# Performance work log

Hardware: AMD Instinct MI355X
Metric: run time of the kernel (lower is better)

Reference implementation:

```python
import jax, jax.numpy as jnp
import numpy as np

B, N, D = 8, 2048, 768
H = 12
HD = D // H
W = 16          # window_size
HOP = 8         # hop_size
GB = N // 2 + 1   # global freq bins = 1025
LB = W // 2 + 1   # local freq bins = 9
NW = (N - W) // HOP + 1  # num windows = 255
EPS_LN = 1e-5


def setup_inputs() -> dict:
    key = jax.random.key(0)
    ks = jax.random.split(key, 12)
    s = 0.02
    return {
        "x": jax.random.normal(ks[0], (B, N, D), dtype=jnp.float32),
        "base_filter_global": jnp.ones((H, GB, 1), jnp.float32),
        "base_filter_local": jnp.ones((H, LB, 1), jnp.float32),
        "modrelu_bias_global": jnp.full((H, GB, 1), -0.1, jnp.float32),
        "modrelu_bias_local": jnp.full((H, LB, 1), -0.1, jnp.float32),
        "w1g": jax.random.normal(ks[1], (D, D), jnp.float32) * s,
        "b1g": jnp.zeros((D,), jnp.float32),
        "w2g": jax.random.normal(ks[2], (D, H * GB), jnp.float32) * s,
        "b2g": jnp.zeros((H * GB,), jnp.float32),
        "w1l": jax.random.normal(ks[3], (D, D), jnp.float32) * s,
        "b1l": jnp.zeros((D,), jnp.float32),
        "w2l": jax.random.normal(ks[4], (D, H * LB), jnp.float32) * s,
        "b2l": jnp.zeros((H * LB,), jnp.float32),
        "fusion_w": jax.random.normal(ks[5], (2,), jnp.float32) * 0.5,
        "ln_gamma": jnp.ones((D,), jnp.float32),
        "ln_beta": jnp.zeros((D,), jnp.float32),
    }


def _modrelu(z, bias):
    # modReLU: ReLU(|z| + b) * z / |z|  (|z| clamped at 1e-6 in denominator)
    a = jnp.abs(z)
    return z * (jax.nn.relu(a + bias) / jnp.maximum(a, 1e-6))


def _hann(w):
    # torch.hann_window default (periodic=True)
    n = jnp.arange(w, dtype=jnp.float32)
    return 0.5 * (1.0 - jnp.cos(2.0 * jnp.pi * n / w))


def reference(x, base_filter_global, base_filter_local, modrelu_bias_global,
              modrelu_bias_local, w1g, b1g, w2g, b2g, w1l, b1l, w2l, b2l,
              fusion_w, ln_gamma, ln_beta):
    b, n, d = x.shape
    x_heads = x.reshape(b, n, H, HD).transpose(0, 2, 1, 3)  # (B,H,N,hd)

    # ---- global branch ----
    Fg = jnp.fft.rfft(x_heads, axis=2, norm='ortho')  # (B,H,GB,hd) complex
    ctx = x.mean(axis=1)  # (B,D)
    mg = jnp.tanh(jax.nn.gelu(ctx @ w1g + b1g, approximate=False) @ w2g + b2g)
    mg = mg.reshape(b, H, GB, 1)
    Fg = Fg * (base_filter_global[None] + mg)
    Fg = _modrelu(Fg, modrelu_bias_global[None])
    x_global = jnp.fft.irfft(Fg, n=n, axis=2, norm='ortho')  # (B,H,N,hd)

    # ---- local (STFT) branch ----
    idx = jnp.arange(NW)[:, None] * HOP + jnp.arange(W)[None, :]  # (NW,W)
    x_win = x_heads[:, :, idx, :]  # (B,H,NW,W,hd)
    w = _hann(W)[None, None, None, :, None]
    x_win = x_win * w
    Fl = jnp.fft.rfft(x_win, axis=3, norm='ortho')  # (B,H,NW,LB,hd)
    ml = jnp.tanh(jax.nn.gelu(ctx @ w1l + b1l, approximate=False) @ w2l + b2l)
    ml = ml.reshape(b, H, 1, LB, 1)
    Fl = Fl * (base_filter_local[None, :, None] + ml)
    Fl = _modrelu(Fl, modrelu_bias_local[None, :, None])
    x_lwin = jnp.fft.irfft(Fl, n=W, axis=3, norm='ortho') * w  # (B,H,NW,W,hd)

    # vectorized overlap-add
    flat_idx = idx.reshape(-1)  # (NW*W,)
    x_local = jnp.zeros((b, H, n, HD), x.dtype).at[:, :, flat_idx, :].add(
        x_lwin.reshape(b, H, NW * W, HD))

    # ---- fuse + residual + layernorm ----
    fused = x_global * fusion_w[0] + x_local * fusion_w[1]  # Linear(2,1,bias=False)
    x_out = fused.transpose(0, 2, 1, 3).reshape(b, n, d)
    y = x + x_out  # dropout is identity at p=0 / eval
    mu = y.mean(axis=-1, keepdims=True)
    var = y.var(axis=-1, keepdims=True)
    return (y - mu) / jnp.sqrt(var + EPS_LN) * ln_gamma + ln_beta
```

## Files before the change

kernel.cpp:

```cpp
#include <hip/hip_runtime.h>
#include <math.h>

#define B_  8
#define N_  2048
#define D_  768
#define H_  12
#define HD_ 64
#define GB_ 1025
#define LB_ 9
#define NW_ 255

#define CBX(i) ((i) + ((i) >> 4))
#define TWX(i) ((i) + ((i) >> 4))

#define C1_ 0.92387953251128674f
#define S1_ 0.38268343236508978f
#define R2_ 0.70710678118654752f

#define FBF(i,k,wr,wi) { const float ar=yr[i],ai=yi[i],br=yr[k],bi=yi[k]; \
  yr[i]=ar+br; yi[i]=ai+bi; const float dr=ar-br, di=ai-bi; \
  yr[k]=fmaf(dr,wr,-(di*(wi))); yi[k]=fmaf(dr,wi,di*(wr)); }
#define FBF1(i,k) { const float ar=yr[i],ai=yi[i],br=yr[k],bi=yi[k]; \
  yr[i]=ar+br; yi[i]=ai+bi; yr[k]=ar-br; yi[k]=ai-bi; }
#define FBFmi(i,k) { const float ar=yr[i],ai=yi[i],br=yr[k],bi=yi[k]; \
  yr[i]=ar+br; yi[i]=ai+bi; yr[k]=ai-bi; yi[k]=br-ar; }

#define IBF(i,k,wr,wi) { const float br=yr[k],bi=yi[k]; \
  const float tr=fmaf(br,wr,-(bi*(wi))), ti=fmaf(br,wi,bi*(wr)); \
  yr[k]=yr[i]-tr; yi[k]=yi[i]-ti; yr[i]+=tr; yi[i]+=ti; }
#define IBF1(i,k) { const float tr=yr[k], ti=yi[k]; \
  yr[k]=yr[i]-tr; yi[k]=yi[i]-ti; yr[i]+=tr; yi[i]+=ti; }
#define IBFpi(i,k) { const float tr=-yi[k], ti=yr[k]; \
  yr[k]=yr[i]-tr; yi[k]=yi[i]-ti; yr[i]+=tr; yi[i]+=ti; }

__device__ __forceinline__ float2 cmulf(float2 a, float2 b) {
  return make_float2(fmaf(a.x, b.x, -(a.y*b.y)), fmaf(a.x, b.y, a.y*b.x));
}
__device__ __forceinline__ float2 csqf(float2 a){ return make_float2(fmaf(a.x,a.x,-(a.y*a.y)), 2.0f*a.x*a.y); }

__device__ __forceinline__ float4 dadd(float4 a, float4 b){ return make_float4(a.x+b.x,a.y+b.y,a.z+b.z,a.w+b.w); }
__device__ __forceinline__ float4 dsub(float4 a, float4 b){ return make_float4(a.x-b.x,a.y-b.y,a.z-b.z,a.w-b.w); }
__device__ __forceinline__ float4 dmul(float4 a, float2 w){
  return make_float4(fmaf(a.x,w.x,-(a.y*w.y)), fmaf(a.x,w.y,a.y*w.x),
                     fmaf(a.z,w.x,-(a.w*w.y)), fmaf(a.z,w.y,a.w*w.x));
}
__device__ __forceinline__ float4 dmulc(float4 a, float2 w){
  return make_float4(fmaf(a.x,w.x,a.y*w.y), fmaf(a.y,w.x,-(a.x*w.y)),
                     fmaf(a.z,w.x,a.w*w.y), fmaf(a.w,w.x,-(a.z*w.y)));
}
__device__ __forceinline__ float4 dmuli(float4 a){
  return make_float4(a.y, -a.x, a.w, -a.z);
}
__device__ __forceinline__ float4 dmulpi(float4 a){
  return make_float4(-a.y, a.x, -a.w, a.z);
}

__device__ __forceinline__ void mr2(float& ar, float& ai, float filt, float bias){
  ar *= filt; ai *= filt;
  const float a = __builtin_amdgcn_sqrtf(fmaf(ar,ar,ai*ai));
  const float s = fmaxf(a + bias, 0.0f) * __builtin_amdgcn_rcpf(fmaxf(a, 1e-6f));
  ar *= s; ai *= s;
}
__device__ __forceinline__ void mr1(float& v, float filt, float bias){
  v *= filt;
  const float a = fabsf(v);
  v *= fmaxf(a + bias, 0.0f) * __builtin_amdgcn_rcpf(fmaxf(a, 1e-6f));
}

template<int S, int L>
__device__ __forceinline__ void fft_trip_fwd(float4* cb, const float2* tw, int j) {
  const int r    = j & (S-1);
  const int base = r + ((j >> L) << (L+3));
  float4 v[8];
  #pragma unroll
  for (int k = 0; k < 8; ++k) v[k] = cb[CBX(base + S*k)];
  const float2 w = tw[TWX(r * (256/S))];
  const float2 c8 = make_float2(R2_, -R2_);
  float2 W1[4];
  W1[0] = w;
  W1[1] = cmulf(w, c8);
  W1[2] = make_float2(w.y, -w.x);
  W1[3] = make_float2(W1[1].y, -W1[1].x);
  #pragma unroll
  for (int k = 0; k < 4; ++k) {
    const float4 u = v[k], t = v[k+4];
    v[k]   = dadd(u, t);
    v[k+4] = dmul(dsub(u, t), W1[k]);
  }
  const float2 w2  = csqf(w);
  const float2 w2i = make_float2(w2.y, -w2.x);
  {
    float4 d;
    d = dsub(v[0], v[2]); v[0] = dadd(v[0], v[2]); v[2] = dmul(d, w2);
    d = dsub(v[1], v[3]); v[1] = dadd(v[1], v[3]); v[3] = dmul(d, w2i);
    d = dsub(v[4], v[6]); v[4] = dadd(v[4], v[6]); v[6] = dmul(d, w2);
    d = dsub(v[5], v[7]); v[5] = dadd(v[5], v[7]); v[7] = dmul(d, w2i);
  }
  const float2 w4 = csqf(w2);
  #pragma unroll
  for (int k = 0; k < 8; k += 2) {
    const float4 d = dsub(v[k], v[k+1]);
    v[k]   = dadd(v[k], v[k+1]);
    v[k+1] = dmul(d, w4);
  }
  #pragma unroll
  for (int k = 0; k < 8; ++k) cb[CBX(base + S*k)] = v[k];
}

__device__ __forceinline__ void fft_trip4_fwd(float4* cb, int j) {
  const int base = j << 3;
  float4 v[8];
  #pragma unroll
  for (int k = 0; k < 8; ++k) v[k] = cb[CBX(base + k)];
  float4 d;
  d = dsub(v[0], v[2]); v[0] = dadd(v[0], v[2]); v[2] = d;
  d = dsub(v[1], v[3]); v[1] = dadd(v[1], v[3]); v[3] = dmuli(d);
  d = dsub(v[4], v[6]); v[4] = dadd(v[4], v[6]); v[6] = d;
  d = dsub(v[5], v[7]); v[5] = dadd(v[5], v[7]); v[7] = dmuli(d);
  #pragma unroll
  for (int k = 0; k < 8; k += 2) {
    d = dsub(v[k], v[k+1]);
    v[k]   = dadd(v[k], v[k+1]);
    v[k+1] = d;
  }
  #pragma unroll
  for (int k = 0; k < 8; ++k) cb[CBX(base + k)] = v[k];
}

__device__ __forceinline__ void fft_trip1_inv(float4* cb, int j) {
  const int base = j << 3;
  float4 v[8];
  #pragma unroll
  for (int k = 0; k < 8; ++k) v[k] = cb[CBX(base + k)];
  #pragma unroll
  for (int k = 0; k < 8; k += 2) {
    const float4 t = v[k+1];
    v[k+1] = dsub(v[k], t);
    v[k]   = dadd(v[k], t);
  }
  {
    float4 t;
    t = v[2];          v[2] = dsub(v[0], t); v[0] = dadd(v[0], t);
    t = dmulpi(v[3]);  v[3] = dsub(v[1], t); v[1] = dadd(v[1], t);
    t = v[6];          v[6] = dsub(v[4], t); v[4] = dadd(v[4], t);
    t = dmulpi(v[7]);  v[7] = dsub(v[5], t); v[5] = dadd(v[5], t);
  }
  #pragma unroll
  for (int k = 0; k < 8; ++k) cb[CBX(base + k)] = v[k];
}

template<int S, int L>
__device__ __forceinline__ void fft_trip_inv(float4* cb, const float2* tw, int j) {
  const int r    = j & (S-1);
  const int base = r + ((j >> L) << (L+3));
  float4 v[8];
  #pragma unroll
  for (int k = 0; k < 8; ++k) v[k] = cb[CBX(base + S*k)];
  const float2 w  = tw[TWX(r * (256/S))];
  const float2 w2 = csqf(w);
  const float2 w4 = csqf(w2);
  #pragma unroll
  for (int k = 0; k < 8; k += 2) {
    const float4 t = dmulc(v[k+1], w4);
    v[k+1] = dsub(v[k], t);
    v[k]   = dadd(v[k], t);
  }
  {
    float4 t;
    t = dmulc(v[2], w2);          v[2] = dsub(v[0], t); v[0] = dadd(v[0], t);
    t = dmulpi(dmulc(v[3], w2));  v[3] = dsub(v[1], t); v[1] = dadd(v[1], t);
    t = dmulc(v[6], w2);          v[6] = dsub(v[4], t); v[4] = dadd(v[4], t);
    t = dmulpi(dmulc(v[7], w2));  v[7] = dsub(v[5], t); v[5] = dadd(v[5], t);
  }
  const float2 c8 = make_float2(R2_, -R2_);
  float2 W1[4];
  W1[0] = w;
  W1[1] = cmulf(w, c8);
  W1[2] = make_float2(w.y, -w.x);
  W1[3] = make_float2(W1[1].y, -W1[1].x);
  #pragma unroll
  for (int k = 0; k < 4; ++k) {
    const float4 t = dmulc(v[k+4], W1[k]);
    v[k+4] = dsub(v[k], t);
    v[k]   = dadd(v[k], t);
  }
  #pragma unroll
  for (int k = 0; k < 8; ++k) cb[CBX(base + S*k)] = v[k];
}

template<int HALF>
__device__ __forceinline__ void local_path(const float4* cb, const float* lf, const float* lb,
                                           int tid, float* w1a, float* w2a) {
  const float HWIN[16] = {0.0f, 0.038060233744356624f, 0.14644660940672624f, 0.30865828381745508f,
                          0.5f, 0.69134171618254492f, 0.85355339059327376f, 0.96193976625564337f,
                          1.0f, 0.96193976625564337f, 0.85355339059327376f, 0.69134171618254492f,
                          0.5f, 0.30865828381745508f, 0.14644660940672624f, 0.038060233744356624f};
  if (tid < NW_) {
    float yr[16], yi[16];
    #pragma unroll
    for (int t = 0; t < 16; ++t) {
      const float4 v = cb[CBX(tid*8 + t)];
      yr[t] = (HALF ? v.z : v.x) * HWIN[t];
      yi[t] = (HALF ? v.w : v.y) * HWIN[t];
    }
    FBF1(0,8); FBF(1,9,C1_,-S1_); FBF(2,10,R2_,-R2_); FBF(3,11,S1_,-C1_);
    FBFmi(4,12); FBF(5,13,-S1_,-C1_); FBF(6,14,-R2_,-R2_); FBF(7,15,-C1_,-S1_);
    FBF1(0,4); FBF(1,5,R2_,-R2_); FBFmi(2,6); FBF(3,7,-R2_,-R2_);
    FBF1(8,12); FBF(9,13,R2_,-R2_); FBFmi(10,14); FBF(11,15,-R2_,-R2_);
    FBF1(0,2); FBFmi(1,3); FBF1(4,6); FBFmi(5,7);
    FBF1(8,10); FBFmi(9,11); FBF1(12,14); FBFmi(13,15);
    FBF1(0,1); FBF1(2,3); FBF1(4,5); FBF1(6,7);
    FBF1(8,9); FBF1(10,11); FBF1(12,13); FBF1(14,15);
    {
      const int IA[9] = {0,8,4,12,2,10,6,14,1};
      const int IB[9] = {0,15,7,11,3,13,5,9,1};
      #pragma unroll
      for (int l = 0; l <= 8; ++l) {
        const int ia = IA[l], ib = IB[l];
        const float Zar=yr[ia], Zai=yi[ia], Zbr=yr[ib], Zbi=yi[ib];
        float f1r = 0.125f*(Zar+Zbr), f1i = 0.125f*(Zai-Zbi);
        float f2r = 0.125f*(Zai+Zbi), f2i = 0.125f*(Zbr-Zar);
        const float ft = lf[l], bs = lb[l];
        mr2(f1r, f1i, ft, bs);
        mr2(f2r, f2i, ft, bs);
        yr[ia] = f1r - f2i; yi[ia] = f1i + f2r;
        if (l >= 1 && l <= 7) { yr[ib] = f1r + f2i; yi[ib] = f2r - f1i; }
      }
    }
    IBF1(0,1); IBF1(2,3); IBF1(4,5); IBF1(6,7);
    IBF1(8,9); IBF1(10,11); IBF1(12,13); IBF1(14,15);
    IBF1(0,2); IBFpi(1,3); IBF1(4,6); IBFpi(5,7);
    IBF1(8,10); IBFpi(9,11); IBF1(12,14); IBFpi(13,15);
    IBF1(0,4); IBF(1,5,R2_,R2_); IBFpi(2,6); IBF(3,7,-R2_,R2_);
    IBF1(8,12); IBF(9,13,R2_,R2_); IBFpi(10,14); IBF(11,15,-R2_,R2_);
    IBF1(0,8); IBF(1,9,C1_,S1_); IBF(2,10,R2_,R2_); IBF(3,11,S1_,C1_);
    IBFpi(4,12); IBF(5,13,-S1_,C1_); IBF(6,14,-R2_,R2_); IBF(7,15,-C1_,S1_);
    #pragma unroll
    for (int t = 0; t < 16; ++t) {
      const float q = 0.25f * HWIN[t];
      w1a[t] = yr[t] * q;
      w2a[t] = yi[t] * q;
    }
  } else {
    #pragma unroll
    for (int t = 0; t < 16; ++t) { w1a[t] = 0.0f; w2a[t] = 0.0f; }
  }
}

__device__ __forceinline__ void combine_oa(const float* w1a, const float* w2a,
                                           const float (*t1)[8], const float (*t2)[8],
                                           int lane, int wvi, float* r1, float* r2) {
  #pragma unroll
  for (int s = 0; s < 8; ++s) {
    float p1 = __shfl_up(w1a[s+8], 1, 64);
    float p2 = __shfl_up(w2a[s+8], 1, 64);
    if (lane == 0) {
      p1 = wvi ? t1[wvi-1][s] : 0.0f;
      p2 = wvi ? t2[wvi-1][s] : 0.0f;
    }
    r1[s] = w1a[s] + p1;
    r2[s] = w2a[s] + p2;
  }
}

__global__ __launch_bounds__(256) void k_ctx(const float* __restrict__ x,
                                             float* __restrict__ ctx) {
  const int b = blockIdx.x;
  const int nc = blockIdx.y;
  const int tid = threadIdx.x;
  const int n0 = nc * 64;
  for (int c = tid; c < D_; c += 256) {
    float s = 0.0f;
    #pragma unroll 4
    for (int n = 0; n < 64; ++n)
      s += x[((size_t)(b*N_ + n0 + n))*D_ + c];
    atomicAdd(&ctx[b*D_ + c], s);
  }
}

__global__ __launch_bounds__(256) void k_mlp1(
    const float* __restrict__ ctx,
    const float* __restrict__ w1g, const float* __restrict__ b1g,
    const float* __restrict__ w1l, const float* __restrict__ b1l,
    float* __restrict__ h1g, float* __restrict__ h1l) {
  __shared__ float hs[B_*D_];
  __shared__ float red[4][16][33];
  const int tid = threadIdx.x;
  const bool isl = (blockIdx.y != 0);
  const float* w1 = isl ? w1l : w1g;
  const float* b1 = isl ? b1l : b1g;
  float*       h1 = isl ? h1l : h1g;
  const int j0 = (int)blockIdx.x * 64;

  for (int i = tid; i < B_*D_; i += 256) hs[i] = ctx[i] * (1.0f/(float)N_);
  __syncthreads();

  const int jg    = tid & 15;
  const int slice = tid >> 4;
  const int j     = j0 + jg*4;
  float acc[8][4] = {};
  {
    const float4* w14 = (const float4*)w1;
    const int jc = j >> 2;
    const int i0 = slice*48;
    #pragma unroll 4
    for (int ii = 0; ii < 48; ++ii) {
      const int i = i0 + ii;
      const float4 w = w14[(size_t)i*192 + jc];
      #pragma unroll
      for (int b = 0; b < 8; ++b) {
        const float hv = hs[b*D_ + i];
        acc[b][0] = fmaf(hv, w.x, acc[b][0]);
        acc[b][1] = fmaf(hv, w.y, acc[b][1]);
        acc[b][2] = fmaf(hv, w.z, acc[b][2]);
        acc[b][3] = fmaf(hv, w.w, acc[b][3]);
      }
    }
  }
  #pragma unroll
  for (int b = 0; b < 8; ++b) {
    #pragma unroll
    for (int q = 0; q < 4; ++q) {
      float v = acc[b][q];
      v += __shfl_xor(v, 16, 64);
      v += __shfl_xor(v, 32, 64);
      acc[b][q] = v;
    }
  }
  const int wv = tid >> 6;
  if ((tid & 63) < 16) {
    #pragma unroll
    for (int b = 0; b < 8; ++b)
      #pragma unroll
      for (int q = 0; q < 4; ++q)
        red[wv][jg][b*4+q] = acc[b][q];
  }
  __syncthreads();
  for (int s = tid; s < 512; s += 256) {
    const int jg2 = s >> 5;
    const int v2  = s & 31;
    const int b   = v2 >> 2, q = v2 & 3;
    const int jo  = j0 + jg2*4 + q;
    const float sum = red[0][jg2][v2] + red[1][jg2][v2]
                    + red[2][jg2][v2] + red[3][jg2][v2];
    const float v = sum + b1[jo];
    h1[(size_t)b*D_ + jo] = 0.5f * v * (1.0f + erff(v * 0.70710678118654752f));
  }
}

__global__ __launch_bounds__(256) void k_mlp2(
    const float* __restrict__ h1g, const float* __restrict__ h1l,
    const float* __restrict__ w2g, const float* __restrict__ b2g,
    const float* __restrict__ w2l, const float* __restrict__ b2l,
    float* __restrict__ mg, float* __restrict__ ml) {
  __shared__ float hs[B_*D_];
  __shared__ float red[4][16][33];
  const int tid = threadIdx.x;
  const bool isg = (blockIdx.x < 193);
  const float* h1 = isg ? h1g : h1l;
  const float* w2 = isg ? w2g : w2l;
  const float* b2 = isg ? b2g : b2l;
  float*       mo = isg ? mg  : ml;
  const int Jmax = isg ? (H_*GB_) : (H_*LB_);
  const int j0   = isg ? (int)blockIdx.x*64 : ((int)blockIdx.x-193)*64;

  for (int i = tid; i < B_*D_; i += 256) hs[i] = h1[i];
  __syncthreads();

  const int jg    = tid & 15;
  const int slice = tid >> 4;
  const int j     = j0 + jg*4;
  float acc[8][4] = {};
  if (j < Jmax) {
    const float4* w24 = (const float4*)w2;
    const int jc   = j >> 2;
    const int rowq = Jmax >> 2;
    const int i0   = slice*48;
    #pragma unroll 4
    for (int ii = 0; ii < 48; ++ii) {
      const int i = i0 + ii;
      const float4 w = w24[(size_t)i*rowq + jc];
      #pragma unroll
      for (int b = 0; b < 8; ++b) {
        const float hv = hs[b*D_ + i];
        acc[b][0] = fmaf(hv, w.x, acc[b][0]);
        acc[b][1] = fmaf(hv, w.y, acc[b][1]);
        acc[b][2] = fmaf(hv, w.z, acc[b][2]);
        acc[b][3] = fmaf(hv, w.w, acc[b][3]);
      }
    }
  }
  #pragma unroll
  for (int b = 0; b < 8; ++b) {
    #pragma unroll
    for (int q = 0; q < 4; ++q) {
      float v = acc[b][q];
      v += __shfl_xor(v, 16, 64);
      v += __shfl_xor(v, 32, 64);
      acc[b][q] = v;
    }
  }
  const int wv = tid >> 6;
  if ((tid & 63) < 16) {
    #pragma unroll
    for (int b = 0; b < 8; ++b)
      #pragma unroll
      for (int q = 0; q < 4; ++q)
        red[wv][jg][b*4+q] = acc[b][q];
  }
  __syncthreads();
  for (int s = tid; s < 512; s += 256) {
    const int jg2 = s >> 5;
    const int v2  = s & 31;
    const int b   = v2 >> 2, q = v2 & 3;
    const int jo  = j0 + jg2*4 + q;
    if (jo < Jmax) {
      const float sum = red[0][jg2][v2] + red[1][jg2][v2]
                      + red[2][jg2][v2] + red[3][jg2][v2];
      mo[(size_t)b*Jmax + jo] = tanhf(sum + b2[jo]);
    }
  }
}

__global__ __launch_bounds__(256) void k_spectral(
    const float* __restrict__ x,
    const float* __restrict__ bfg, const float* __restrict__ bfl,
    const float* __restrict__ mbg, const float* __restrict__ mbl,
    const float* __restrict__ mg,  const float* __restrict__ ml,
    const float* __restrict__ fw,  float* __restrict__ fused) {
  __shared__ float4 cb[N_ + (N_>>4)];
  __shared__ float2 tw[256 + 16];
  __shared__ float  t1b[2][4][8], t2b[2][4][8];
  __shared__ float  lf[LB_], lb[LB_];

  const int tid = threadIdx.x;
  const int id  = blockIdx.x;
  const int v_  = (id & 7) * 192 + (id >> 3);
  const int dq  = v_ & 15;
  const int bh  = v_ >> 4;
  const int h   = bh % H_;
  const int b   = bh / H_;
  const int d   = dq * 4;
  const int c   = h*HD_ + d;
  const int col0 = bh*HD_ + d;

  {
    float s_, c_;
    sincospif(-(float)tid * (1.0f/1024.0f), &s_, &c_);
    tw[TWX(tid)] = make_float2(c_, s_);
  }
  if (tid < LB_) {
    lf[tid] = bfl[h*LB_ + tid] + ml[(size_t)b*(H_*LB_) + h*LB_ + tid];
    lb[tid] = mbl[h*LB_ + tid];
  }
  for (int n = tid; n < N_; n += 256) {
    cb[CBX(n)] = *(const float4*)&x[((size_t)(b*N_ + n))*D_ + c];
  }
  __syncthreads();

  const int lane = tid & 63, wvi = tid >> 6;
  float r1[8], r2[8], r3[8], r4[8];
  {
    float w1a[16], w2a[16];
    local_path<0>(cb, lf, lb, tid, w1a, w2a);
    if (lane == 63 && tid < NW_) {
      #pragma unroll
      for (int s = 0; s < 8; ++s) { t1b[0][wvi][s] = w1a[8+s]; t2b[0][wvi][s] = w2a[8+s]; }
    }
    __syncthreads();
    combine_oa(w1a, w2a, t1b[0], t2b[0], lane, wvi, r1, r2);
  }
  {
    float w1a[16], w2a[16];
    local_path<1>(cb, lf, lb, tid, w1a, w2a);
    if (lane == 63 && tid < NW_) {
      #pragma unroll
      for (int s = 0; s < 8; ++s) { t1b[1][wvi][s] = w1a[8+s]; t2b[1][wvi][s] = w2a[8+s]; }
    }
    __syncthreads();
    combine_oa(w1a, w2a, t1b[1], t2b[1], lane, wvi, r3, r4);
  }

  fft_trip_fwd<256,8>(cb, tw, tid); __syncthreads();
  fft_trip_fwd< 32,5>(cb, tw, tid); __syncthreads();
  fft_trip_fwd<  4,2>(cb, tw, tid); __syncthreads();
  fft_trip4_fwd(cb, tid);           __syncthreads();

  const float fsc = 0.022097086912079610f;
  {
    const float* mgp = mg + (size_t)b*(H_*GB_) + h*GB_;
    const float* bfp = bfg + h*GB_;
    const float* mbp = mbg + h*GB_;
    const int kb = (tid & 192) + (int)(__brev((unsigned)(tid & 63)) >> 26);
    #pragma unroll
    for (int t = 0; t < 4; ++t) {
      const int k = kb + 256*t;
      if (k == 0) {
        float4 Z0 = cb[CBX(0)], Zn = cb[CBX(1)];
        const float f0t = bfp[0] + mgp[0],     b0 = mbp[0];
        const float fnt = bfp[1024] + mgp[1024], bn = mbp[1024];
        float a0 = Z0.x*fsc, a1 = Z0.y*fsc, a2 = Z0.z*fsc, a3 = Z0.w*fsc;
        mr1(a0, f0t, b0); mr1(a1, f0t, b0); mr1(a2, f0t, b0); mr1(a3, f0t, b0);
        cb[CBX(0)] = make_float4(a0, a1, a2, a3);
        float n0v = Zn.x*fsc, n1v = Zn.y*fsc, n2v = Zn.z*fsc, n3v = Zn.w*fsc;
        mr1(n0v, fnt, bn); mr1(n1v, fnt, bn); mr1(n2v, fnt, bn); mr1(n3v, fnt, bn);
        cb[CBX(1)] = make_float4(n0v, n1v, n2v, n3v);
      } else {
        const int ik  = (int)(__brev((unsigned)k) >> 21);
        const int imk = (int)(__brev((unsigned)(2048 - k)) >> 21);
        const float4 Za = cb[CBX(ik)], Zb = cb[CBX(imk)];
        const float hs_ = 0.5f * fsc;
        const float filt = bfp[k] + mgp[k], bias = mbp[k];
        float f1r = (Za.x + Zb.x) * hs_, f1i = (Za.y - Zb.y) * hs_;
        float f2r = (Za.y + Zb.y) * hs_, f2i = (Zb.x - Za.x) * hs_;
        mr2(f1r, f1i, filt, bias);
        mr2(f2r, f2i, filt, bias);
        float g1r = (Za.z + Zb.z) * hs_, g1i = (Za.w - Zb.w) * hs_;
        float g2r = (Za.w + Zb.w) * hs_, g2i = (Zb.z - Za.z) * hs_;
        mr2(g1r, g1i, filt, bias);
        mr2(g2r, g2i, filt, bias);
        cb[CBX(ik)]  = make_float4(f1r - f2i, f1i + f2r, g1r - g2i, g1i + g2r);
        cb[CBX(imk)] = make_float4(f1r + f2i, f2r - f1i, g1r + g2i, g2r - g1i);
      }
    }
  }
  __syncthreads();

  fft_trip1_inv(cb, tid);           __syncthreads();
  fft_trip_inv<  4,2>(cb, tw, tid); __syncthreads();
  fft_trip_inv< 32,5>(cb, tw, tid); __syncthreads();
  fft_trip_inv<256,8>(cb, tw, tid); __syncthreads();

  const float fw1v = fw[1];
  const float fwg  = fw[0] * fsc;
  float* f0 = fused + (size_t)col0 * N_;
  float* f1p = f0 + N_;
  float* f2p = f0 + 2*N_;
  float* f3p = f0 + 3*N_;
  const int n0 = tid * 8;
  float v0[8], v1[8], v2[8], v3[8];
  #pragma unroll
  for (int s = 0; s < 8; ++s) {
    const float4 g = cb[CBX(n0 + s)];
    v0[s] = fwg * g.x + fw1v * r1[s];
    v1[s] = fwg * g.y + fw1v * r2[s];
    v2[s] = fwg * g.z + fw1v * r3[s];
    v3[s] = fwg * g.w + fw1v * r4[s];
  }
  *(float4*)&f0[n0]    = make_float4(v0[0], v0[1], v0[2], v0[3]);
  *(float4*)&f0[n0+4]  = make_float4(v0[4], v0[5], v0[6], v0[7]);
  *(float4*)&f1p[n0]   = make_float4(v1[0], v1[1], v1[2], v1[3]);
  *(float4*)&f1p[n0+4] = make_float4(v1[4], v1[5], v1[6], v1[7]);
  *(float4*)&f2p[n0]   = make_float4(v2[0], v2[1], v2[2], v2[3]);
  *(float4*)&f2p[n0+4] = make_float4(v2[4], v2[5], v2[6], v2[7]);
  *(float4*)&f3p[n0]   = make_float4(v3[0], v3[1], v3[2], v3[3]);
  *(float4*)&f3p[n0+4] = make_float4(v3[4], v3[5], v3[6], v3[7]);
}

__global__ __launch_bounds__(256) void k_ln(const float* __restrict__ x,
                                            const float* __restrict__ fused,
                                            const float* __restrict__ gamma,
                                            const float* __restrict__ beta,
                                            float* __restrict__ out) {
  __shared__ float yt[16*776];
  __shared__ float mus[16], rsd[16];
  const int bi = blockIdx.x;
  const int b  = bi >> 7;
  const int n0 = (bi & 127) * 16;
  const int tid = threadIdx.x;

  {
    const float4* x4 = (const float4*)(x + ((size_t)(b*N_ + n0))*D_);
    for (int i = tid; i < 16*D_/4; i += 256) {
      const int nn = i / 192, r = i - nn*192;
      const float4 v = x4[i];
      float* yp = &yt[nn*776 + r*4];
      yp[0] = v.x; yp[1] = v.y; yp[2] = v.z; yp[3] = v.w;
    }
  }
  __syncthreads();
  {
    const float4* fu4 = (const float4*)fused;
    for (int i = tid; i < 16*D_/4; i += 256) {
      const int cc = i >> 2, q = (i & 3) * 4;
      const float4 g = fu4[(((size_t)(b*D_ + cc))*N_ + n0)/4 + (i & 3)];
      yt[(q+0)*776 + cc] += g.x;
      yt[(q+1)*776 + cc] += g.y;
      yt[(q+2)*776 + cc] += g.z;
      yt[(q+3)*776 + cc] += g.w;
    }
  }
  __syncthreads();
  const int nn = tid >> 4, cl = tid & 15;
  float s1 = 0.0f, s2 = 0.0f;
  for (int c = cl; c < D_; c += 16) {
    const float v = yt[nn*776 + c];
    s1 += v; s2 += v*v;
  }
  #pragma unroll
  for (int m = 8; m >= 1; m >>= 1) {
    s1 += __shfl_xor(s1, m, 16);
    s2 += __shfl_xor(s2, m, 16);
  }
  if (cl == 0) {
    const float mu  = s1 * (1.0f/(float)D_);
    const float var = s2 * (1.0f/(float)D_) - mu*mu;
    mus[nn] = mu;
    rsd[nn] = rsqrtf(var + 1e-5f);
  }
  __syncthreads();
  {
    float4* o4 = (float4*)(out + ((size_t)(b*N_ + n0))*D_);
    const float4* g4 = (const float4*)gamma;
    const float4* be4 = (const float4*)beta;
    for (int i = tid; i < 16*D_/4; i += 256) {
      const int nn2 = i / 192, r = i - nn2*192;
      const float mu = mus[nn2], rs = rsd[nn2];
      const float4 gm = g4[r], bt = be4[r];
      const float* yp = &yt[nn2*776 + r*4];
      float4 o;
      o.x = (yp[0] - mu) * rs * gm.x + bt.x;
      o.y = (yp[1] - mu) * rs * gm.y + bt.y;
      o.z = (yp[2] - mu) * rs * gm.z + bt.z;
      o.w = (yp[3] - mu) * rs * gm.w + bt.w;
      o4[i] = o;
    }
  }
}

extern "C" void kernel_launch(void* const* d_in, const int* in_sizes, int n_in,
                              void* d_out, int out_size, void* d_ws, size_t ws_size,
                              hipStream_t stream) {
  const float* x   = (const float*)d_in[0];
  const float* bfg = (const float*)d_in[1];
  const float* bfl = (const float*)d_in[2];
  const float* mbg = (const float*)d_in[3];
  const float* mbl = (const float*)d_in[4];
  const float* w1g = (const float*)d_in[5];
  const float* b1g = (const float*)d_in[6];
  const float* w2g = (const float*)d_in[7];
  const float* b2g = (const float*)d_in[8];
  const float* w1l = (const float*)d_in[9];
  const float* b1l = (const float*)d_in[10];
  const float* w2l = (const float*)d_in[11];
  const float* b2l = (const float*)d_in[12];
  const float* fw  = (const float*)d_in[13];
  const float* gam = (const float*)d_in[14];
  const float* bet = (const float*)d_in[15];
  float* out = (float*)d_out;

  float* ws    = (float*)d_ws;
  float* ctx   = ws;
  float* h1g   = ws + 6144;
  float* h1l   = ws + 12288;
  float* mg    = ws + 18432;
  float* ml    = ws + 116832;
  float* fused = ws + 117696;

  hipMemsetAsync(ctx, 0, (size_t)B_*D_*sizeof(float), stream);
  k_ctx<<<dim3(B_, 32), 256, 0, stream>>>(x, ctx);
  k_mlp1<<<dim3(12, 2), 256, 0, stream>>>(ctx, w1g, b1g, w1l, b1l, h1g, h1l);
  k_mlp2<<<195, 256, 0, stream>>>(h1g, h1l, w2g, b2g, w2l, b2l, mg, ml);
  k_spectral<<<B_*H_*16, 256, 0, stream>>>(x, bfg, bfl, mbg, mbl, mg, ml, fw, fused);
  k_ln<<<B_*N_/16, 256, 0, stream>>>(x, fused, gam, bet, out);
}
```

Measured before the change: 287.0 us.

## Interleave fused buffer as float4 columns and split MLP1 across batch

```diff
diff --git a/kernel.cpp b/kernel.cpp
--- a/kernel.cpp
+++ b/kernel.cpp
@@ -283,22 +283,23 @@
     const float* __restrict__ w1g, const float* __restrict__ b1g,
     const float* __restrict__ w1l, const float* __restrict__ b1l,
     float* __restrict__ h1g, float* __restrict__ h1l) {
-  __shared__ float hs[B_*D_];
-  __shared__ float red[4][16][33];
+  __shared__ float hs[D_];
+  __shared__ float red[4][16][5];
   const int tid = threadIdx.x;
   const bool isl = (blockIdx.y != 0);
+  const int bb = blockIdx.z;
   const float* w1 = isl ? w1l : w1g;
   const float* b1 = isl ? b1l : b1g;
   float*       h1 = isl ? h1l : h1g;
   const int j0 = (int)blockIdx.x * 64;
 
-  for (int i = tid; i < B_*D_; i += 256) hs[i] = ctx[i] * (1.0f/(float)N_);
+  for (int i = tid; i < D_; i += 256) hs[i] = ctx[bb*D_ + i] * (1.0f/(float)N_);
   __syncthreads();
 
   const int jg    = tid & 15;
   const int slice = tid >> 4;
   const int j     = j0 + jg*4;
-  float acc[8][4] = {};
+  float acc[4] = {};
   {
     const float4* w14 = (const float4*)w1;
     const int jc = j >> 2;
@@ -307,44 +308,35 @@
     for (int ii = 0; ii < 48; ++ii) {
       const int i = i0 + ii;
       const float4 w = w14[(size_t)i*192 + jc];
-      #pragma unroll
-      for (int b = 0; b < 8; ++b) {
-        const float hv = hs[b*D_ + i];
-        acc[b][0] = fmaf(hv, w.x, acc[b][0]);
-        acc[b][1] = fmaf(hv, w.y, acc[b][1]);
-        acc[b][2] = fmaf(hv, w.z, acc[b][2]);
-        acc[b][3] = fmaf(hv, w.w, acc[b][3]);
-      }
-    }
-  }
-  #pragma unroll
-  for (int b = 0; b < 8; ++b) {
-    #pragma unroll
-    for (int q = 0; q < 4; ++q) {
-      float v = acc[b][q];
-      v += __shfl_xor(v, 16, 64);
-      v += __shfl_xor(v, 32, 64);
-      acc[b][q] = v;
-    }
+      const float hv = hs[i];
+      acc[0] = fmaf(hv, w.x, acc[0]);
+      acc[1] = fmaf(hv, w.y, acc[1]);
+      acc[2] = fmaf(hv, w.z, acc[2]);
+      acc[3] = fmaf(hv, w.w, acc[3]);
+    }
+  }
+  #pragma unroll
+  for (int q = 0; q < 4; ++q) {
+    float v = acc[q];
+    v += __shfl_xor(v, 16, 64);
+    v += __shfl_xor(v, 32, 64);
+    acc[q] = v;
   }
   const int wv = tid >> 6;
   if ((tid & 63) < 16) {
     #pragma unroll
-    for (int b = 0; b < 8; ++b)
-      #pragma unroll
-      for (int q = 0; q < 4; ++q)
-        red[wv][jg][b*4+q] = acc[b][q];
-  }
-  __syncthreads();
-  for (int s = tid; s < 512; s += 256) {
-    const int jg2 = s >> 5;
-    const int v2  = s & 31;
-    const int b   = v2 >> 2, q = v2 & 3;
+    for (int q = 0; q < 4; ++q)
+      red[wv][jg][q] = acc[q];
+  }
+  __syncthreads();
+  if (tid < 64) {
+    const int jg2 = tid >> 2;
+    const int q   = tid & 3;
     const int jo  = j0 + jg2*4 + q;
-    const float sum = red[0][jg2][v2] + red[1][jg2][v2]
-                    + red[2][jg2][v2] + red[3][jg2][v2];
+    const float sum = red[0][jg2][q] + red[1][jg2][q]
+                    + red[2][jg2][q] + red[3][jg2][q];
     const float v = sum + b1[jo];
-    h1[(size_t)b*D_ + jo] = 0.5f * v * (1.0f + erff(v * 0.70710678118654752f));
+    h1[(size_t)bb*D_ + jo] = 0.5f * v * (1.0f + erff(v * 0.70710678118654752f));
   }
 }
 
@@ -442,7 +434,7 @@
   const int b   = bh / H_;
   const int d   = dq * 4;
   const int c   = h*HD_ + d;
-  const int col0 = bh*HD_ + d;
+  const int cg  = bh*16 + dq;
 
   {
     float s_, c_;
@@ -533,28 +525,16 @@
 
   const float fw1v = fw[1];
   const float fwg  = fw[0] * fsc;
-  float* f0 = fused + (size_t)col0 * N_;
-  float* f1p = f0 + N_;
-  float* f2p = f0 + 2*N_;
-  float* f3p = f0 + 3*N_;
+  float4* fo = (float4*)fused + (size_t)cg * N_;
   const int n0 = tid * 8;
-  float v0[8], v1[8], v2[8], v3[8];
   #pragma unroll
   for (int s = 0; s < 8; ++s) {
     const float4 g = cb[CBX(n0 + s)];
-    v0[s] = fwg * g.x + fw1v * r1[s];
-    v1[s] = fwg * g.y + fw1v * r2[s];
-    v2[s] = fwg * g.z + fw1v * r3[s];
-    v3[s] = fwg * g.w + fw1v * r4[s];
-  }
-  *(float4*)&f0[n0]    = make_float4(v0[0], v0[1], v0[2], v0[3]);
-  *(float4*)&f0[n0+4]  = make_float4(v0[4], v0[5], v0[6], v0[7]);
-  *(float4*)&f1p[n0]   = make_float4(v1[0], v1[1], v1[2], v1[3]);
-  *(float4*)&f1p[n0+4] = make_float4(v1[4], v1[5], v1[6], v1[7]);
-  *(float4*)&f2p[n0]   = make_float4(v2[0], v2[1], v2[2], v2[3]);
-  *(float4*)&f2p[n0+4] = make_float4(v2[4], v2[5], v2[6], v2[7]);
-  *(float4*)&f3p[n0]   = make_float4(v3[0], v3[1], v3[2], v3[3]);
-  *(float4*)&f3p[n0+4] = make_float4(v3[4], v3[5], v3[6], v3[7]);
+    fo[n0 + s] = make_float4(fwg * g.x + fw1v * r1[s],
+                             fwg * g.y + fw1v * r2[s],
+                             fwg * g.z + fw1v * r3[s],
+                             fwg * g.w + fw1v * r4[s]);
+  }
 }
 
 __global__ __launch_bounds__(256) void k_ln(const float* __restrict__ x,
@@ -581,13 +561,11 @@
   __syncthreads();
   {
     const float4* fu4 = (const float4*)fused;
-    for (int i = tid; i < 16*D_/4; i += 256) {
-      const int cc = i >> 2, q = (i & 3) * 4;
-      const float4 g = fu4[(((size_t)(b*D_ + cc))*N_ + n0)/4 + (i & 3)];
-      yt[(q+0)*776 + cc] += g.x;
-      yt[(q+1)*776 + cc] += g.y;
-      yt[(q+2)*776 + cc] += g.z;
-      yt[(q+3)*776 + cc] += g.w;
+    for (int i = tid; i < 16*192; i += 256) {
+      const int cgl = i >> 4, rn = i & 15;
+      const float4 g = fu4[((size_t)(b*192 + cgl))*N_ + n0 + rn];
+      float* yp = &yt[rn*776 + cgl*4];
+      yp[0] += g.x; yp[1] += g.y; yp[2] += g.z; yp[3] += g.w;
     }
   }
   __syncthreads();
@@ -659,7 +637,7 @@
 
   hipMemsetAsync(ctx, 0, (size_t)B_*D_*sizeof(float), stream);
   k_ctx<<<dim3(B_, 32), 256, 0, stream>>>(x, ctx);
-  k_mlp1<<<dim3(12, 2), 256, 0, stream>>>(ctx, w1g, b1g, w1l, b1l, h1g, h1l);
+  k_mlp1<<<dim3(12, 2, 8), 256, 0, stream>>>(ctx, w1g, b1g, w1l, b1l, h1g, h1l);
   k_mlp2<<<195, 256, 0, stream>>>(h1g, h1l, w2g, b2g, w2l, b2l, mg, ml);
   k_spectral<<<B_*H_*16, 256, 0, stream>>>(x, bfg, bfl, mbg, mbl, mg, ml, fw, fused);
   k_ln<<<B_*N_/16, 256, 0, stream>>>(x, fused, gam, bet, out);
```

After: 279.9 us. -2.5%, faster.
